# Optimization experiments

Hardware: AMD Instinct MI355X
Metric: run time of the kernel (lower is better)

The kernel has to match this reference:

```python
import jax, jax.numpy as jnp
import numpy as np

N_EVENTS = 50000
TS_SIZE = 512
N_NEURONS = 256
LAMBDA_HOMEO = 0.25


def setup_inputs() -> dict:
    key = jax.random.key(0)
    k1, k2 = jax.random.split(key)
    # event time surfaces (nonnegative, like torch surfaces)
    all_ts = jax.random.uniform(k1, (N_EVENTS, TS_SIZE), dtype=jnp.float32)
    # synapses.weight ~ U[0,1), as in torch.nn.init.uniform_(a=0,b=1)
    W = jax.random.uniform(k2, (N_NEURONS, TS_SIZE), dtype=jnp.float32)
    cumhisto = jnp.ones((N_NEURONS,), dtype=jnp.float32)
    return {"all_ts": all_ts, "W": W, "cumhisto": cumhisto}


def reference(all_ts, W, cumhisto):
    """Training branch (learning_flag=True, homeo_flag=True) of hotslayer.forward.

    Sequential per-event: normalize ts, cosine-like scores beta, homeostatic gain
    picks the winner, winner row of W is pulled toward ts, histogram incremented.
    Returns (per-event winners [N_EVENTS], final W [N,TS], final cumhisto [N]).
    """
    n_neurons = W.shape[0]

    def step(carry, ts):
        W, ch = carry
        ts = ts / jnp.linalg.norm(ts)
        w_norm = jnp.linalg.norm(W, axis=1)          # [N]
        beta = (W @ ts) / w_norm                      # [N]
        gain = jnp.exp(LAMBDA_HOMEO * (1.0 - n_neurons * ch / ch.sum()))
        n_star = jnp.argmax(gain * beta)
        Ck = W[n_star]                                # [TS]
        alpha = 0.01 / (1.0 + ch[n_star] / 20000.0)
        W = W.at[n_star].set(Ck + alpha * beta[n_star] * (ts - Ck))
        ch = ch.at[n_star].add(1.0)
        return (W, ch), n_star

    (W_f, ch_f), winners = jax.lax.scan(step, (W, cumhisto), all_ts)
    return winners, W_f, ch_f
```

## Files before the change

kernel.cpp:

```cpp
#include <hip/hip_runtime.h>
#include <hip/hip_bf16.h>

#define N_EVENTS 50000
#define TS 512
#define NN 256
#define BATCH 512
#define SUB 64
#define LAMB 0.25f
#define NB 98

#define RLF(v, l) __int_as_float(__builtin_amdgcn_readlane(__float_as_int(v), (l)))
#define RLI(v, l) __builtin_amdgcn_readlane((v), (l))
#define FRCP(x) __builtin_amdgcn_rcpf(x)
#define FRSQ(x) __builtin_amdgcn_rsqf(x)
#define DPP_MAXF(x, ctrl)                                                            \
    { int _s = __builtin_amdgcn_update_dpp(__float_as_int(x), __float_as_int(x),     \
                                           (ctrl), 0xF, 0xF, false);                 \
      (x) = fmaxf((x), __int_as_float(_s)); }

typedef unsigned long long u64;


__global__ __launch_bounds__(256)
void inv_kernel(const float* __restrict__ ts, float* __restrict__ inv)
{
    __shared__ double red[256];
    const int e = blockIdx.x;
    const int d = threadIdx.x;
    const float* row = ts + (size_t)e * TS;
    float x0 = row[d], x1 = row[d + 256];
    red[d] = (double)x0 * x0 + (double)x1 * x1;
    __syncthreads();
    for (int st = 128; st > 0; st >>= 1) {
        if (d < st) red[d] += red[d + st];
        __syncthreads();
    }
    if (d == 0) inv[e] = (float)(1.0 / sqrt(red[0]));
}

__global__ __launch_bounds__(256)
void init_kernel(const float* __restrict__ chin, float* __restrict__ ch,
                 float* Pn0, float* Pn1, float* phi0, float* phi1,
                 float* c0, float* c1, float* d0, float* d1,
                 int* w0, int* w1)
{
    int i = blockIdx.x * 256 + threadIdx.x;
    if (i < NN) { ch[i] = chin[i]; Pn0[i] = 1.f; Pn1[i] = 1.f; }
    if (i < BATCH) {
        phi0[i] = 0.f; phi1[i] = 0.f; c0[i] = 0.f; c1[i] = 0.f;
        d0[i] = 0.f; d1[i] = 0.f; w0[i] = 0; w1[i] = 0;
    }
}


__device__ void gram_tile(float* SH, const float* __restrict__ ts,
                          const float* __restrict__ inv,
                          int astart, int as, int bstart2, int bs2,
                          int be, int bf, float* __restrict__ outp, int transpose)
{
    float* At = SH;
    float* Bt = SH + 64 * 33;
    if (be * 64 >= as || bf * 64 >= bs2) return;
    const int tx = threadIdx.x & 15, ty = threadIdx.x >> 4;
    float acc[4][4] = {};
    for (int kt = 0; kt < TS; kt += 32) {
        for (int it = threadIdx.x; it < 64 * 32; it += 256) {
            int r = it >> 5, c = it & 31;
            int ra = be * 64 + r, rb = bf * 64 + r;
            At[r * 33 + c] = (ra < as) ? ts[(size_t)(astart + ra) * TS + kt + c] : 0.f;
            Bt[r * 33 + c] = (rb < bs2) ? ts[(size_t)(bstart2 + rb) * TS + kt + c] : 0.f;
        }
        __syncthreads();
#pragma unroll
        for (int kk = 0; kk < 32; ++kk) {
            float av[4], bv[4];
#pragma unroll
            for (int i = 0; i < 4; ++i) av[i] = At[(ty * 4 + i) * 33 + kk];
#pragma unroll
            for (int j = 0; j < 4; ++j) bv[j] = Bt[(tx * 4 + j) * 33 + kk];
#pragma unroll
            for (int i = 0; i < 4; ++i)
#pragma unroll
                for (int j = 0; j < 4; ++j)
                    acc[i][j] += av[i] * bv[j];
        }
        __syncthreads();
    }
#pragma unroll
    for (int i = 0; i < 4; ++i) {
        int e = be * 64 + ty * 4 + i;
        if (e >= as) continue;
        float ie = inv[astart + e];
#pragma unroll
        for (int j = 0; j < 4; ++j) {
            int f = bf * 64 + tx * 4 + j;
            if (f >= bs2) continue;
            float v = acc[i][j] * ie * inv[bstart2 + f];
            if (transpose) outp[(size_t)f * BATCH + e] = v;
            else           outp[(size_t)e * BATCH + f] = v;
        }
    }
}

__global__ __launch_bounds__(256)
void gram_kernel(const float* __restrict__ ts, const float* __restrict__ inv,
                 float* __restrict__ outp, int astart, int as, int bstart2, int bs2,
                 int upper, int transpose)
{
    __shared__ float SHg[64 * 33 * 2];
    if (upper && (int)blockIdx.y < (int)blockIdx.x) return;
    gram_tile(SHg, ts, inv, astart, as, bstart2, bs2, blockIdx.x, blockIdx.y,
              outp, transpose);
}


__device__ void neuron_body(float* shf, double* red,
    const float* __restrict__ ts, const float* __restrict__ inv,
    const float* __restrict__ Wsrc, float* __restrict__ wdst,
    const int* __restrict__ winPrev, const float* __restrict__ phiPrev,
    const float* __restrict__ PnPrev,
    float* __restrict__ wn2W, float* __restrict__ S2W,
    const float* __restrict__ chbuf, float* __restrict__ chout,
    int n, int bprev_start, int bs_prev, int bnext_start, int bs_next)
{
    int* winS = (int*)shf;
    float* phiS = shf + 512;
    float* WL = shf + 1024;
    const int d = threadIdx.x;
    for (int i = d; i < bs_prev; i += 256) { winS[i] = winPrev[i]; phiS[i] = phiPrev[i]; }
    __syncthreads();
    const float Pf = PnPrev[n];
    float w0 = Wsrc[n * TS + d];
    float w1 = Wsrc[n * TS + d + 256];
    double a0 = 0.0, a1 = 0.0;
    for (int e = 0; e < bs_prev; ++e) {
        if (winS[e] == n) {
            double coef = (double)phiS[e];
            float iv = inv[bprev_start + e];
            const float* tr = ts + (size_t)(bprev_start + e) * TS;
            a0 += coef * (double)(tr[d] * iv);
            a1 += coef * (double)(tr[d + 256] * iv);
        }
    }
    w0 = (float)((double)Pf * ((double)w0 + a0));
    w1 = (float)((double)Pf * ((double)w1 + a1));
    wdst[n * TS + d] = w0;
    wdst[n * TS + d + 256] = w1;
    WL[d] = w0; WL[d + 256] = w1;
    if (wn2W) {
        red[d] = (double)w0 * w0 + (double)w1 * w1;
        __syncthreads();
        for (int st = 128; st > 0; st >>= 1) {
            if (d < st) red[d] += red[d + st];
            __syncthreads();
        }
        if (d == 0) wn2W[n] = (float)red[0];
    } else {
        __syncthreads();
    }
    if (bs_next > 0) {
#pragma unroll
        for (int rep = 0; rep < 2; ++rep) {
            int f = d + rep * 256;
            if (f < bs_next) {
                double acc = 0.0;
                const float* tr = ts + (size_t)(bnext_start + f) * TS;
                for (int k = 0; k < TS; ++k) acc += (double)tr[k] * (double)WL[k];
                S2W[f * NN + n] = (float)(acc * (double)inv[bnext_start + f]);
            }
        }
    }
    if (chout && d == 0) chout[n] = chbuf[n];
}

__global__ __launch_bounds__(256)
void neuron_kernel(const float* __restrict__ ts, const float* __restrict__ inv,
    const float* __restrict__ Wsrc, float* __restrict__ wdst,
    const int* __restrict__ winPrev, const float* __restrict__ phiPrev,
    const float* __restrict__ PnPrev,
    float* __restrict__ wn2W, float* __restrict__ S2W,
    const float* __restrict__ chbuf, float* __restrict__ chout,
    int bprev_start, int bs_prev, int bnext_start, int bs_next)
{
    __shared__ float SHN[1536];
    __shared__ double redN[256];
    neuron_body(SHN, redN, ts, inv, Wsrc, wdst, winPrev, phiPrev, PnPrev,
                wn2W, S2W, chbuf, chout, blockIdx.x,
                bprev_start, bs_prev, bnext_start, bs_next);
}


__global__ __launch_bounds__(256)
void fix_kernel(const float* __restrict__ S2r, const float* __restrict__ GxTr,
    const int* __restrict__ winPrev, const float* __restrict__ phiPrev,
    const float* __restrict__ cPrev, const float* __restrict__ dPrev,
    const float* __restrict__ PnPrev, const float* __restrict__ wn2b,
    float* __restrict__ S0corr, float* __restrict__ wn2start,
    int bs, int b0flag)
{
    __shared__ int winS[512];
    __shared__ float phiP[512];
    __shared__ float gr[512];
    __shared__ float cS[512];
    __shared__ float dS[512];
    const int tid = threadIdx.x;
    const int f = blockIdx.x;
    for (int i = tid; i < 512; i += 256) {
        int w = winPrev[i];
        winS[i] = w;
        phiP[i] = b0flag ? 0.f : phiPrev[i] * PnPrev[w];
        cS[i] = cPrev[i];
        dS[i] = dPrev[i];
        gr[i] = (b0flag || f >= bs) ? 0.f : GxTr[(size_t)f * BATCH + i];
    }
    __syncthreads();
    if (f < bs) {
        int n = tid;
        float acc = PnPrev[n] * S2r[f * NN + n];
        if (!b0flag) {
            for (int e = 0; e < 512; ++e)
                if (winS[e] == n) acc += phiP[e] * gr[e];
        }
        S0corr[f * NN + n] = acc;
    }
    if (f == 0 && tid < 64) {
        const int lane = tid;
        float w2[4];
#pragma unroll
        for (int k = 0; k < 4; ++k) w2[k] = wn2b[k * 64 + lane];
        for (int e = 0; e < 512; ++e) {
            float c = cS[e];
            if (c != 0.f) {
                int w = winS[e];
                int owner = w & 63, kk = w >> 6;
                float omc = 1.f - c;
                float t2 = 2.f * c * omc * dS[e] + c * c;
#pragma unroll
                for (int k = 0; k < 4; ++k)
                    if (lane == owner && k == kk) w2[k] = omc * omc * w2[k] + t2;
            }
        }
#pragma unroll
        for (int k = 0; k < 4; ++k) wn2start[k * 64 + lane] = w2[k];
    }
}


__device__ void block0_body(float* SH,
    const float* __restrict__ S0corr, const float* __restrict__ GwR,
    const float* __restrict__ wn2start, float* __restrict__ chbuf,
    int* __restrict__ winCur, float* __restrict__ phiCur,
    float* __restrict__ cCur, float* __restrict__ dotCur, float* __restrict__ PnCur,
    float* __restrict__ winners_out, int bstart, int bs)
{
    float* ACC = SH;
    float* GS  = SH + 16384;
    float* GL  = SH + 20480;
    int*   winL = (int*)(SH + 24576);
    float* phiL = SH + 25088;
    float* cL   = SH + 25600;
    float* dL   = SH + 26112;

    const int tid = threadIdx.x, wid = tid >> 6, lane = tid & 63;

    const float KC = -(LAMB * 256.0f * 1.44269504f);
    float ch0 = 0, ch1 = 0, ch2 = 0, ch3 = 0;
    float w20 = 1, w21 = 1, w22 = 1, w23 = 1;
    float rn0 = 1, rn1 = 1, rn2 = 1, rn3 = 1;
    float Pn0 = 1, Pn1 = 1, Pn2 = 1, Pn3 = 1;
    float Sbase = 1.f;
    if (wid == 0) {
        ch0 = chbuf[lane];        ch1 = chbuf[64 + lane];
        ch2 = chbuf[128 + lane];  ch3 = chbuf[192 + lane];
        w20 = wn2start[lane];       w21 = wn2start[64 + lane];
        w22 = wn2start[128 + lane]; w23 = wn2start[192 + lane];
        rn0 = FRSQ(w20); rn1 = FRSQ(w21); rn2 = FRSQ(w22); rn3 = FRSQ(w23);
        float loc = ch0 + ch1 + ch2 + ch3;
#pragma unroll
        for (int off = 32; off > 0; off >>= 1) loc += __shfl_xor(loc, off, 64);
        Sbase = loc;
    }

    const int nsub = (bs + SUB - 1) >> 6;
    for (int sub = 0; sub < nsub; ++sub) {
        const int s0 = sub << 6;
        const int cnt = min(SUB, bs - s0);
        __syncthreads();
        {
            const int n = tid;
            for (int f = 0; f < cnt; f += 8) {
                const float* src = S0corr + (size_t)(s0 + f) * NN + n;
                float v0 = src[0 * NN], v1 = src[1 * NN], v2 = src[2 * NN], v3 = src[3 * NN];
                float v4 = src[4 * NN], v5 = src[5 * NN], v6 = src[6 * NN], v7 = src[7 * NN];
                ACC[(f + 0) * NN + ((n + f + 0) & 255)] = v0;
                ACC[(f + 1) * NN + ((n + f + 1) & 255)] = v1;
                ACC[(f + 2) * NN + ((n + f + 2) & 255)] = v2;
                ACC[(f + 3) * NN + ((n + f + 3) & 255)] = v3;
                ACC[(f + 4) * NN + ((n + f + 4) & 255)] = v4;
                ACC[(f + 5) * NN + ((n + f + 5) & 255)] = v5;
                ACC[(f + 6) * NN + ((n + f + 6) & 255)] = v6;
                ACC[(f + 7) * NN + ((n + f + 7) & 255)] = v7;
            }
        }
        for (int it = tid; it < SUB * SUB; it += 256) {
            int t = it >> 6, f = it & 63;
            GS[it] = (t < cnt && f < cnt) ? GwR[(size_t)(s0 + t) * BATCH + s0 + f] : 0.f;
        }
        for (int base = 0; base < s0; base += 64) {
            {
                const int i0 = tid, i1 = tid + 256, i2 = tid + 512, i3 = tid + 768;
                for (int rep = 0; rep < 4096; rep += 1024) {
                    float g0 = GwR[(size_t)(base + ((i0 + rep) >> 6)) * BATCH + s0 + (i0 & 63)];
                    float g1 = GwR[(size_t)(base + ((i1 + rep) >> 6)) * BATCH + s0 + (i1 & 63)];
                    float g2 = GwR[(size_t)(base + ((i2 + rep) >> 6)) * BATCH + s0 + (i2 & 63)];
                    float g3 = GwR[(size_t)(base + ((i3 + rep) >> 6)) * BATCH + s0 + (i3 & 63)];
                    GL[i0 + rep] = g0; GL[i1 + rep] = g1;
                    GL[i2 + rep] = g2; GL[i3 + rep] = g3;
                }
            }
            int wreg = winL[base + lane];
            float preg = phiL[base + lane];
            __syncthreads();
            for (int j = 0; j < 64; ++j) {
                int wj = RLI(wreg, j);
                if ((wj & 3) == wid) {
                    float pj = RLF(preg, j);
                    if (lane < cnt)
                        ACC[lane * NN + ((wj + lane) & 255)] += pj * GL[j * 64 + lane];
                }
            }
            __syncthreads();
        }
        __syncthreads();

        if (wid == 0) {
            float a0 = ACC[(lane) & 255];
            float a1 = ACC[(64 + lane) & 255];
            float a2 = ACC[(128 + lane) & 255];
            float a3 = ACC[(192 + lane) & 255];

            for (int t = 0; t < cnt; ++t) {
                const int ib = s0 + t;
                const float Kk2 = KC * FRCP(Sbase + (float)ib);
                const bool hn = (t + 1 < cnt);
                const float g1v = GS[t * SUB + ((t + 1) & 63)];
                float n0 = 0.f, n1 = 0.f, n2 = 0.f, n3 = 0.f;
                if (hn) {
                    const int r = t + 1;
                    n0 = ACC[r * NN + ((lane + r) & 255)];
                    n1 = ACC[r * NN + ((64 + lane + r) & 255)];
                    n2 = ACC[r * NN + ((128 + lane + r) & 255)];
                    n3 = ACC[r * NN + ((192 + lane + r) & 255)];
                }
                const int fo = t + 1 + lane;
                const float gval = GS[t * SUB + (fo & 63)];

                const float pa0 = Pn0 * a0, pa1 = Pn1 * a1;
                const float pa2 = Pn2 * a2, pa3 = Pn3 * a3;
                const float b0 = pa0 * rn0, b1 = pa1 * rn1;
                const float b2 = pa2 * rn2, b3 = pa3 * rn3;
                const float k0 = b0 * exp2f(Kk2 * ch0);
                const float k1 = b1 * exp2f(Kk2 * ch1);
                const float k2 = b2 * exp2f(Kk2 * ch2);
                const float k3 = b3 * exp2f(Kk2 * ch3);

                u64 K  = ((u64)(unsigned)__float_as_uint(k0) << 32) | (unsigned)(255 - lane);
                u64 T1 = ((u64)(unsigned)__float_as_uint(k1) << 32) | (unsigned)(191 - lane);
                u64 T2 = ((u64)(unsigned)__float_as_uint(k2) << 32) | (unsigned)(127 - lane);
                u64 T3 = ((u64)(unsigned)__float_as_uint(k3) << 32) | (unsigned)(63 - lane);
                if (T1 > K) K = T1;
                if (T2 > K) K = T2;
                if (T3 > K) K = T3;
#define DPPSTEP(ctrl)                                                              \
                { int _hi = (int)(K >> 32), _lo = (int)(unsigned)K;                 \
                  int _shi = __builtin_amdgcn_update_dpp(_hi, _hi, (ctrl), 0xF, 0xF, false); \
                  int _slo = __builtin_amdgcn_update_dpp(_lo, _lo, (ctrl), 0xF, 0xF, false); \
                  u64 _S = ((u64)(unsigned)_shi << 32) | (unsigned)_slo;           \
                  if (_S > K) K = _S; }
                DPPSTEP(0x111) DPPSTEP(0x112) DPPSTEP(0x114)
                DPPSTEP(0x118) DPPSTEP(0x142) DPPSTEP(0x143)
#undef DPPSTEP
                const int loAll = __builtin_amdgcn_ds_bpermute(63 << 2, (int)(unsigned)K);
                const int ns = 255 - (loAll & 0xFF);
                const int ksq = ns >> 6, owner = ns & 63;

                const float bsel  = (ksq == 0) ? b0  : (ksq == 1) ? b1  : (ksq == 2) ? b2  : b3;
                const float pasel = (ksq == 0) ? pa0 : (ksq == 1) ? pa1 : (ksq == 2) ? pa2 : pa3;
                const float Psel  = (ksq == 0) ? Pn0 : (ksq == 1) ? Pn1 : (ksq == 2) ? Pn2 : Pn3;
                const float csel  = (ksq == 0) ? ch0 : (ksq == 1) ? ch1 : (ksq == 2) ? ch2 : ch3;
                const int oaddr = owner << 2;
                const float betas = __int_as_float(__builtin_amdgcn_ds_bpermute(oaddr, __float_as_int(bsel)));
                const float pas   = __int_as_float(__builtin_amdgcn_ds_bpermute(oaddr, __float_as_int(pasel)));
                const float pold  = __int_as_float(__builtin_amdgcn_ds_bpermute(oaddr, __float_as_int(Psel)));
                const float chs   = __int_as_float(__builtin_amdgcn_ds_bpermute(oaddr, __float_as_int(csel)));

                const float alpha = 0.01f * FRCP(1.0f + chs * (1.0f / 20000.0f));
                const float c    = alpha * betas;
                const float omc  = 1.0f - c;
                const float pnew = pold * omc;
                const float phi  = c * FRCP(pnew);

                const bool lo_own = (lane == owner);
                if (lo_own && ksq == 0) { w20 = omc * omc * w20 + 2.f * c * omc * pas + c * c;
                    rn0 = FRSQ(w20); ch0 += 1.f; Pn0 = pnew; n0 += phi * g1v; }
                if (lo_own && ksq == 1) { w21 = omc * omc * w21 + 2.f * c * omc * pas + c * c;
                    rn1 = FRSQ(w21); ch1 += 1.f; Pn1 = pnew; n1 += phi * g1v; }
                if (lo_own && ksq == 2) { w22 = omc * omc * w22 + 2.f * c * omc * pas + c * c;
                    rn2 = FRSQ(w22); ch2 += 1.f; Pn2 = pnew; n2 += phi * g1v; }
                if (lo_own && ksq == 3) { w23 = omc * omc * w23 + 2.f * c * omc * pas + c * c;
                    rn3 = FRSQ(w23); ch3 += 1.f; Pn3 = pnew; n3 += phi * g1v; }

                if (lane == 0) {
                    winL[ib] = ns; phiL[ib] = phi;
                    cL[ib] = c; dL[ib] = pas;
                }
                if (lane > 0 && fo < cnt)
                    ACC[fo * NN + ((ns + fo) & 255)] += phi * gval;

                if (hn) { a0 = n0; a1 = n1; a2 = n2; a3 = n3; }
            }
        }
    }
    __syncthreads();
    if (wid == 0) {
        chbuf[lane] = ch0;        chbuf[64 + lane] = ch1;
        chbuf[128 + lane] = ch2;  chbuf[192 + lane] = ch3;
        PnCur[lane] = Pn0;        PnCur[64 + lane] = Pn1;
        PnCur[128 + lane] = Pn2;  PnCur[192 + lane] = Pn3;
    }
    for (int i = tid; i < bs; i += 256) {
        int w = winL[i];
        winCur[i] = w;
        phiCur[i] = phiL[i];
        cCur[i] = cL[i];
        dotCur[i] = dL[i];
        winners_out[bstart + i] = (float)w;
    }
}


__global__ __launch_bounds__(256)
void fusedA_kernel(const float* __restrict__ ts, const float* __restrict__ inv,
    const float* __restrict__ S0corr, const float* __restrict__ GwR,
    float* __restrict__ GwW, float* __restrict__ GxTW,
    const float* __restrict__ wn2start, float* __restrict__ chbuf,
    const int* __restrict__ winPrev, const float* __restrict__ phiPrev,
    const float* __restrict__ PnPrev,
    int* __restrict__ winCur, float* __restrict__ phiCur,
    float* __restrict__ cCur, float* __restrict__ dotCur, float* __restrict__ PnCur,
    float* __restrict__ Wcur, float* __restrict__ wn2W, float* __restrict__ S2W,
    float* __restrict__ out, int b, int bstart, int bs, int bnext_start, int bs_next)
{
    __shared__ float SH[26656];
    const int bx = blockIdx.x;
    if (bx == 0) {
        block0_body(SH, S0corr, GwR, wn2start, chbuf,
                    winCur, phiCur, cCur, dotCur, PnCur, out, bstart, bs);
    } else if (bx <= NN) {
        neuron_body(SH, (double*)(SH + 1536), ts, inv, Wcur, Wcur,
                    winPrev, phiPrev, PnPrev, wn2W, S2W, nullptr, nullptr,
                    bx - 1, bstart - BATCH, (b == 0) ? 0 : BATCH,
                    bnext_start, bs_next);
    } else {
        int job = bx - (NN + 1);
        if (bs_next <= 0) return;
        if (job < 64) {
            gram_tile(SH, ts, inv, bstart, bs, bnext_start, bs_next,
                      job >> 3, job & 7, GxTW, 1);
        } else {
            int jw = job - 64;
            int be = 0;
            while (jw >= 8 - be) { jw -= 8 - be; ++be; }
            int bf = be + jw;
            gram_tile(SH, ts, inv, bnext_start, bs_next, bnext_start, bs_next,
                      be, bf, GwW, 0);
        }
    }
}


__global__ __launch_bounds__(256)
void winit_kernel(const float* __restrict__ Wcur, const float* __restrict__ chin,
                  float* __restrict__ ch, float* __restrict__ wn2, float* __restrict__ rn)
{
    __shared__ double red[256];
    const int n = blockIdx.x;
    const int d = threadIdx.x;
    float w0 = Wcur[n * TS + d], w1 = Wcur[n * TS + d + 256];
    red[d] = (double)w0 * w0 + (double)w1 * w1;
    __syncthreads();
    for (int st = 128; st > 0; st >>= 1) {
        if (d < st) red[d] += red[d + st];
        __syncthreads();
    }
    if (d == 0) {
        double s = red[0];
        wn2[n] = (float)s;
        rn[n]  = (float)(1.0 / sqrt(s));
        ch[n]  = chin[n];
    }
}

__global__ __launch_bounds__(256)
void s0_gemm_kernel(const float* __restrict__ ts, const float* __restrict__ Wcur,
                    const float* __restrict__ inv, float* __restrict__ S0P,
                    int bstart, int bs)
{
    __shared__ float At[64][33];
    __shared__ float Bt[64][33];
    const int bf = blockIdx.x;
    const int bn = blockIdx.y;
    if (bf * 64 >= bs) return;
    const int tx = threadIdx.x & 15, ty = threadIdx.x >> 4;
    double acc[4][4] = {};
    for (int kt = 0; kt < TS; kt += 32) {
        for (int it = threadIdx.x; it < 64 * 32; it += 256) {
            int r = it >> 5, c = it & 31;
            int row = bf * 64 + r;
            At[r][c] = (row < bs) ? ts[(size_t)(bstart + row) * TS + kt + c] : 0.f;
            Bt[r][c] = Wcur[(bn * 64 + r) * TS + kt + c];
        }
        __syncthreads();
#pragma unroll
        for (int kk = 0; kk < 32; ++kk) {
            float av[4], bv[4];
#pragma unroll
            for (int i = 0; i < 4; ++i) av[i] = At[ty * 4 + i][kk];
#pragma unroll
            for (int j = 0; j < 4; ++j) bv[j] = Bt[tx * 4 + j][kk];
#pragma unroll
            for (int i = 0; i < 4; ++i)
#pragma unroll
                for (int j = 0; j < 4; ++j)
                    acc[i][j] += (double)av[i] * (double)bv[j];
        }
        __syncthreads();
    }
#pragma unroll
    for (int i = 0; i < 4; ++i) {
        int f = bf * 64 + ty * 4 + i;
        if (f >= bs) continue;
        double iv = (double)inv[bstart + f];
#pragma unroll
        for (int j = 0; j < 4; ++j) {
            int n = bn * 64 + tx * 4 + j;
            S0P[f * NN + n] = (float)(acc[i][j] * iv);
        }
    }
}

__global__ __launch_bounds__(256)
void seq_step_kernel(const float* __restrict__ S0P, const float* __restrict__ Gb,
                     float* __restrict__ ch_g, const float* __restrict__ wn2_g,
                     const float* __restrict__ rn_g, float* __restrict__ Pn_g,
                     float* __restrict__ phi_g, int* __restrict__ win_g,
                     float* __restrict__ winners_out, int bstart, int bs)
{
    __shared__ float ACC[SUB * NN];
    __shared__ float GS[SUB * SUB];
    __shared__ float GL[SUB * SUB];
    __shared__ int   winL[BATCH];
    __shared__ float phiL[BATCH];

    const int tid = threadIdx.x;
    const int wid = tid >> 6;
    const int lane = tid & 63;

    float ch[4] = {0, 0, 0, 0}, wn2v[4] = {1, 1, 1, 1};
    float rn[4] = {1, 1, 1, 1}, Pn[4] = {1, 1, 1, 1};
    float Ssum = 1.f, sinv = 1.f;
    if (wid == 0) {
#pragma unroll
        for (int k = 0; k < 4; ++k) {
            int n = k * 64 + lane;
            ch[k]   = ch_g[n];
            wn2v[k] = wn2_g[n];
            rn[k]   = rn_g[n];
            Pn[k]   = 1.0f;
        }
        float loc = ch[0] + ch[1] + ch[2] + ch[3];
#pragma unroll
        for (int off = 32; off > 0; off >>= 1) loc += __shfl_xor(loc, off, 64);
        Ssum = loc;
        sinv = 1.0f / Ssum;
    }

    const int nsub = (bs + SUB - 1) >> 6;
    for (int sub = 0; sub < nsub; ++sub) {
        const int s0 = sub << 6;
        const int cnt = min(SUB, bs - s0);
        __syncthreads();

        for (int it = tid; it < cnt * NN; it += 256) {
            int r = it >> 8, n = it & 255;
            ACC[r * NN + ((n + r) & 255)] = S0P[(s0 + r) * NN + n];
        }
        for (int it = tid; it < cnt * SUB; it += 256) {
            int t = it >> 6, f = it & 63;
            GS[t * SUB + f] = (f < cnt) ? Gb[(s0 + t) * BATCH + s0 + f] : 0.f;
        }
        __syncthreads();

        for (int base = 0; base < s0; base += 64) {
            for (int it = tid; it < 64 * 64; it += 256)
                GL[it] = Gb[(base + (it >> 6)) * BATCH + s0 + (it & 63)];
            int   wreg = winL[base + lane];
            float preg = phiL[base + lane];
            __syncthreads();
            for (int j = 0; j < 64; ++j) {
                int wj = RLI(wreg, j);
                if ((wj & 3) == wid) {
                    float pj = RLF(preg, j);
                    if (lane < cnt)
                        ACC[lane * NN + ((wj + lane) & 255)] += pj * GL[j * 64 + lane];
                }
            }
            __syncthreads();
        }

        if (wid == 0) {
            float acur[4];
#pragma unroll
            for (int k = 0; k < 4; ++k) acur[k] = ACC[(k * 64 + lane) & 255];

            for (int t = 0; t < cnt; ++t) {
                const bool havenext = (t + 1 < cnt);
                float anext[4] = {0.f, 0.f, 0.f, 0.f};
                if (havenext) {
                    const int r = t + 1;
#pragma unroll
                    for (int k = 0; k < 4; ++k)
                        anext[k] = ACC[r * NN + ((k * 64 + lane + r) & 255)];
                }
                const int forig = t + 1 + lane;
                const float gval = GS[t * SUB + (forig & 63)];

                const float gmul = 256.0f * sinv;
                float beta[4], key[4];
                float kmax;
#pragma unroll
                for (int k = 0; k < 4; ++k) {
                    float dot = Pn[k] * acur[k];
                    beta[k] = dot * rn[k];
                    float frac = ch[k] * gmul;
                    float gain = __expf(LAMB * (1.0f - frac));
                    key[k] = gain * beta[k];
                }
                kmax = fmaxf(fmaxf(key[0], key[1]), fmaxf(key[2], key[3]));
                DPP_MAXF(kmax, 0x111); DPP_MAXF(kmax, 0x112); DPP_MAXF(kmax, 0x114);
                DPP_MAXF(kmax, 0x118); DPP_MAXF(kmax, 0x142); DPP_MAXF(kmax, 0x143);
                const float smax = RLF(kmax, 63);

                unsigned long long m0 = __ballot(key[0] == smax);
                unsigned long long m1 = __ballot(key[1] == smax);
                unsigned long long m2 = __ballot(key[2] == smax);
                unsigned long long m3 = __ballot(key[3] == smax);
                int ns = m0 ? (int)__builtin_ctzll(m0)
                       : m1 ? 64  + (int)__builtin_ctzll(m1)
                       : m2 ? 128 + (int)__builtin_ctzll(m2)
                            : 192 + (int)__builtin_ctzll(m3);
                ns = __builtin_amdgcn_readfirstlane(ns);
                const int owner = ns & 63, ks = ns >> 6;

                float bsel = (ks == 0) ? beta[0] : (ks == 1) ? beta[1] : (ks == 2) ? beta[2] : beta[3];
                float csel = (ks == 0) ? ch[0]   : (ks == 1) ? ch[1]   : (ks == 2) ? ch[2]   : ch[3];
                float asel = (ks == 0) ? acur[0] : (ks == 1) ? acur[1] : (ks == 2) ? acur[2] : acur[3];
                float psel = (ks == 0) ? Pn[0]   : (ks == 1) ? Pn[1]   : (ks == 2) ? Pn[2]   : Pn[3];
                const float betas = RLF(bsel, owner);
                const float chs   = RLF(csel, owner);
                const float dots  = RLF(psel * asel, owner);
                const float pold  = RLF(psel, owner);

                const float alpha = 0.01f / (1.0f + chs / 20000.0f);
                const float c    = alpha * betas;
                const float omc  = 1.0f - c;
                const float pnew = pold * omc;
                const float phi  = c / pnew;
                const float g1   = RLF(gval, 0);

#pragma unroll
                for (int k = 0; k < 4; ++k) {
                    bool me = (lane == owner) && (k == ks);
                    if (me) {
                        wn2v[k] = omc * omc * wn2v[k] + 2.f * c * omc * dots + c * c;
                        rn[k] = 1.0f / sqrtf(wn2v[k]);
                        ch[k] += 1.0f;
                        Pn[k] = pnew;
                        anext[k] += phi * g1;
                    }
                }
                if (lane > 0 && forig < cnt)
                    ACC[forig * NN + ((ns + forig) & 255)] += phi * gval;

                const int ib = s0 + t;
                if (lane == 0) {
                    winL[ib] = ns; phiL[ib] = phi;
                    win_g[ib] = ns; phi_g[ib] = phi;
                    winners_out[bstart + ib] = (float)ns;
                }
                Ssum += 1.0f;
                sinv = 1.0f / Ssum;
                if (havenext) {
#pragma unroll
                    for (int k = 0; k < 4; ++k) acur[k] = anext[k];
                }
            }
        }
        __syncthreads();
    }

    if (wid == 0) {
#pragma unroll
        for (int k = 0; k < 4; ++k) {
            int n = k * 64 + lane;
            ch_g[n] = ch[k];
            Pn_g[n] = Pn[k];
        }
    }
}

__global__ __launch_bounds__(256)
void wupdate_kernel(const float* __restrict__ ts, const float* __restrict__ inv,
                    const int* __restrict__ win_g, const float* __restrict__ phi_g,
                    const float* __restrict__ Pn_g, float* __restrict__ Wcur,
                    float* __restrict__ wn2_g, float* __restrict__ rn_g,
                    int bstart, int bs)
{
    __shared__ int   winS[BATCH];
    __shared__ float phiS[BATCH];
    __shared__ double red[256];
    const int n = blockIdx.x;
    const int d = threadIdx.x;
    for (int i = d; i < bs; i += 256) { winS[i] = win_g[i]; phiS[i] = phi_g[i]; }
    __syncthreads();
    const float Pf = Pn_g[n];
    float w0 = Wcur[n * TS + d];
    float w1 = Wcur[n * TS + d + 256];
    double a0 = 0.0, a1 = 0.0;
    for (int ib = 0; ib < bs; ++ib) {
        if (winS[ib] == n) {
            double coef = (double)phiS[ib] * (double)Pf;
            float iv = inv[bstart + ib];
            const float* tr = ts + (size_t)(bstart + ib) * TS;
            a0 += coef * (double)(tr[d] * iv);
            a1 += coef * (double)(tr[d + 256] * iv);
        }
    }
    w0 = (float)((double)Pf * (double)w0 + a0);
    w1 = (float)((double)Pf * (double)w1 + a1);
    Wcur[n * TS + d] = w0;
    Wcur[n * TS + d + 256] = w1;
    red[d] = (double)w0 * w0 + (double)w1 * w1;
    __syncthreads();
    for (int st = 128; st > 0; st >>= 1) {
        if (d < st) red[d] += red[d + st];
        __syncthreads();
    }
    if (d == 0) {
        double s = red[0];
        wn2_g[n] = (float)s;
        rn_g[n]  = (float)(1.0 / sqrt(s));
    }
}

__global__ __launch_bounds__(256)
void final_kernel(const float* __restrict__ Wcur, const float* __restrict__ ch,
                  float* __restrict__ out)
{
    int i = blockIdx.x * 256 + threadIdx.x;
    if (i < NN * TS) out[N_EVENTS + i] = Wcur[i];
    else if (i < NN * TS + NN) out[N_EVENTS + i] = ch[i - NN * TS];
}


extern "C" void kernel_launch(void* const* d_in, const int* in_sizes, int n_in,
                              void* d_out, int out_size, void* d_ws, size_t ws_size,
                              hipStream_t stream)
{
    const float* ts   = (const float*)d_in[0];
    const float* W0   = (const float*)d_in[1];
    const float* chin = (const float*)d_in[2];
    float* out = (float*)d_out;
    float* ws  = (float*)d_ws;

    const size_t FULL_FLOATS = 1628544;
    if (ws_size >= FULL_FLOATS * sizeof(float)) {
        float* inv  = ws + 0;
        float* Wcur = ws + 50048;
        float* ch   = ws + 181120;
        float* wn2b[2] = { ws + 181376, ws + 181632 };
        float* wn2s = ws + 181888;
        float* Pn[2]  = { ws + 182144, ws + 182400 };
        float* phi[2] = { ws + 182656, ws + 183168 };
        float* cE[2]  = { ws + 183680, ws + 184192 };
        float* dE[2]  = { ws + 184704, ws + 185216 };
        int*   win[2] = { (int*)(ws + 185728), (int*)(ws + 186240) };
        float* S2[2]  = { ws + 186752, ws + 317824 };
        float* S0c    = ws + 448896;
        float* GxT[2] = { ws + 579968, ws + 842112 };
        float* Gw[2]  = { ws + 1104256, ws + 1366400 };

        hipMemcpyAsync(Wcur, W0, (size_t)NN * TS * sizeof(float),
                       hipMemcpyDeviceToDevice, stream);
        inv_kernel<<<N_EVENTS, 256, 0, stream>>>(ts, inv);
        init_kernel<<<2, 256, 0, stream>>>(chin, ch, Pn[0], Pn[1], phi[0], phi[1],
                                           cE[0], cE[1], dE[0], dE[1], win[0], win[1]);
        neuron_kernel<<<NN, 256, 0, stream>>>(ts, inv, Wcur, Wcur,
            win[1], phi[1], Pn[1], wn2b[0], S2[0], nullptr, nullptr,
            0, 0, 0, BATCH);
        gram_kernel<<<dim3(8, 8), 256, 0, stream>>>(ts, inv, Gw[0],
            0, BATCH, 0, BATCH, 1, 0);

        for (int b = 0; b < NB; ++b) {
            const int cs = b & 1, ps = 1 - cs;
            const int bstart = b * BATCH;
            const int bs = min(BATCH, N_EVENTS - bstart);
            const int bnext = bstart + BATCH;
            const int bsn = (b == NB - 1) ? 0 : min(BATCH, N_EVENTS - bnext);

            fix_kernel<<<BATCH, 256, 0, stream>>>(S2[cs], GxT[cs],
                win[ps], phi[ps], cE[ps], dE[ps], Pn[ps], wn2b[cs],
                S0c, wn2s, bs, (b == 0) ? 1 : 0);

            const int grid = (b == NB - 1) ? (NN + 1) : (NN + 1 + 100);
            fusedA_kernel<<<grid, 256, 0, stream>>>(ts, inv, S0c, Gw[cs],
                Gw[ps], GxT[ps], wn2s, ch,
                win[ps], phi[ps], Pn[ps],
                win[cs], phi[cs], cE[cs], dE[cs], Pn[cs],
                Wcur, wn2b[ps], S2[ps],
                out, b, bstart, bs, bnext, bsn);
        }
        neuron_kernel<<<NN, 256, 0, stream>>>(ts, inv, Wcur, out + N_EVENTS,
            win[1], phi[1], Pn[1], nullptr, nullptr, ch, out + N_EVENTS + NN * TS,
            97 * BATCH, 336, 0, 0);
    } else {
        float* inv  = ws + 0;
        float* Wcur = ws + 50048;
        float* ch   = ws + 181120;
        float* wn2  = ws + 181376;
        float* rn   = ws + 181632;
        float* Pn   = ws + 181888;
        float* phi  = ws + 182144;
        int*   win  = (int*)(ws + 182656);
        float* S0P  = ws + 183168;
        float* G    = ws + 314240;

        hipMemcpyAsync(Wcur, W0, (size_t)NN * TS * sizeof(float),
                       hipMemcpyDeviceToDevice, stream);
        inv_kernel<<<N_EVENTS, 256, 0, stream>>>(ts, inv);
        winit_kernel<<<NN, 256, 0, stream>>>(Wcur, chin, ch, wn2, rn);

        for (int b = 0; b < NB; ++b) {
            int bstart = b * BATCH;
            int bs = min(BATCH, N_EVENTS - bstart);
            s0_gemm_kernel<<<dim3(8, 4), 256, 0, stream>>>(ts, Wcur, inv, S0P, bstart, bs);
            gram_kernel<<<dim3(8, 8), 256, 0, stream>>>(ts, inv, G,
                bstart, bs, bstart, bs, 1, 0);
            seq_step_kernel<<<1, 256, 0, stream>>>(S0P, G, ch, wn2, rn, Pn, phi, win,
                                                   out, bstart, bs);
            wupdate_kernel<<<NN, 256, 0, stream>>>(ts, inv, win, phi, Pn, Wcur,
                                                   wn2, rn, bstart, bs);
        }
        final_kernel<<<(NN * TS + NN + 255) / 256, 256, 0, stream>>>(Wcur, ch, out);
    }
}
```

Before: 62.64 ms.

## Defer winner state update via top-2 argmax to shorten the serial dependency chain

The sequential winner-selection loop now tracks the top two keys across the wavefront reduction. The previous winner's update (state writeback and ACC propagation) is applied lazily in the next iteration. The previous winner's new key is recomputed separately and merged with the best key among the other neurons. This takes the per-step state update off the critical path between one argmax and the next, so it can overlap with the reduction. In exchange the DPP reduction work doubles, plus an extra bpermute and more registers and branching.

```diff
diff --git a/kernel.cpp b/kernel.cpp
--- a/kernel.cpp
+++ b/kernel.cpp
@@ -334,27 +334,18 @@
         __syncthreads();
 
         if (wid == 0) {
-            float a0 = ACC[(lane) & 255];
-            float a1 = ACC[(64 + lane) & 255];
-            float a2 = ACC[(128 + lane) & 255];
-            float a3 = ACC[(192 + lane) & 255];
+            int   p = 0;
+            float up_phi = 0.f, up_pnew = 1.f, up_w2 = 1.f, up_rn = 1.f, up_ch = 0.f;
+            float bp_a = 0.f, bp_Pn = 1.f, bp_rn = 1.f, bp_ch = 0.f, bp_w2 = 1.f;
 
             for (int t = 0; t < cnt; ++t) {
                 const int ib = s0 + t;
                 const float Kk2 = KC * FRCP(Sbase + (float)ib);
-                const bool hn = (t + 1 < cnt);
-                const float g1v = GS[t * SUB + ((t + 1) & 63)];
-                float n0 = 0.f, n1 = 0.f, n2 = 0.f, n3 = 0.f;
-                if (hn) {
-                    const int r = t + 1;
-                    n0 = ACC[r * NN + ((lane + r) & 255)];
-                    n1 = ACC[r * NN + ((64 + lane + r) & 255)];
-                    n2 = ACC[r * NN + ((128 + lane + r) & 255)];
-                    n3 = ACC[r * NN + ((192 + lane + r) & 255)];
-                }
-                const int fo = t + 1 + lane;
-                const float gval = GS[t * SUB + (fo & 63)];
-
+
+                const float a0 = ACC[t * NN + ((lane + t) & 255)];
+                const float a1 = ACC[t * NN + ((64 + lane + t) & 255)];
+                const float a2 = ACC[t * NN + ((128 + lane + t) & 255)];
+                const float a3 = ACC[t * NN + ((192 + lane + t) & 255)];
                 const float pa0 = Pn0 * a0, pa1 = Pn1 * a1;
                 const float pa2 = Pn2 * a2, pa3 = Pn3 * a3;
                 const float b0 = pa0 * rn0, b1 = pa1 * rn1;
@@ -363,61 +354,105 @@
                 const float k1 = b1 * exp2f(Kk2 * ch1);
                 const float k2 = b2 * exp2f(Kk2 * ch2);
                 const float k3 = b3 * exp2f(Kk2 * ch3);
-
-                u64 K  = ((u64)(unsigned)__float_as_uint(k0) << 32) | (unsigned)(255 - lane);
-                u64 T1 = ((u64)(unsigned)__float_as_uint(k1) << 32) | (unsigned)(191 - lane);
-                u64 T2 = ((u64)(unsigned)__float_as_uint(k2) << 32) | (unsigned)(127 - lane);
-                u64 T3 = ((u64)(unsigned)__float_as_uint(k3) << 32) | (unsigned)(63 - lane);
-                if (T1 > K) K = T1;
-                if (T2 > K) K = T2;
-                if (T3 > K) K = T3;
-#define DPPSTEP(ctrl)                                                              \
-                { int _hi = (int)(K >> 32), _lo = (int)(unsigned)K;                 \
-                  int _shi = __builtin_amdgcn_update_dpp(_hi, _hi, (ctrl), 0xF, 0xF, false); \
-                  int _slo = __builtin_amdgcn_update_dpp(_lo, _lo, (ctrl), 0xF, 0xF, false); \
-                  u64 _S = ((u64)(unsigned)_shi << 32) | (unsigned)_slo;           \
-                  if (_S > K) K = _S; }
-                DPPSTEP(0x111) DPPSTEP(0x112) DPPSTEP(0x114)
-                DPPSTEP(0x118) DPPSTEP(0x142) DPPSTEP(0x143)
-#undef DPPSTEP
-                const int loAll = __builtin_amdgcn_ds_bpermute(63 << 2, (int)(unsigned)K);
-                const int ns = 255 - (loAll & 0xFF);
-                const int ksq = ns >> 6, owner = ns & 63;
+                u64 Q0 = ((u64)(unsigned)__float_as_uint(k0) << 32) | (unsigned)(255 - lane);
+                u64 Q1 = ((u64)(unsigned)__float_as_uint(k1) << 32) | (unsigned)(191 - lane);
+                u64 Q2 = ((u64)(unsigned)__float_as_uint(k2) << 32) | (unsigned)(127 - lane);
+                u64 Q3 = ((u64)(unsigned)__float_as_uint(k3) << 32) | (unsigned)(63 - lane);
+                u64 M1 = Q0, M2 = Q1;
+                if (M2 > M1) { u64 tm = M1; M1 = M2; M2 = tm; }
+                if (Q2 > M1) { M2 = M1; M1 = Q2; } else if (Q2 > M2) M2 = Q2;
+                if (Q3 > M1) { M2 = M1; M1 = Q3; } else if (Q3 > M2) M2 = Q3;
+#define DPPD(ctrl) { \
+    int s1h = __builtin_amdgcn_update_dpp((int)(M1 >> 32), (int)(M1 >> 32), (ctrl), 0xF, 0xF, false); \
+    int s1l = __builtin_amdgcn_update_dpp((int)(unsigned)M1, (int)(unsigned)M1, (ctrl), 0xF, 0xF, false); \
+    int s2h = __builtin_amdgcn_update_dpp((int)(M2 >> 32), (int)(M2 >> 32), (ctrl), 0xF, 0xF, false); \
+    int s2l = __builtin_amdgcn_update_dpp((int)(unsigned)M2, (int)(unsigned)M2, (ctrl), 0xF, 0xF, false); \
+    u64 S1 = ((u64)(unsigned)s1h << 32) | (unsigned)s1l; \
+    u64 S2 = ((u64)(unsigned)s2h << 32) | (unsigned)s2l; \
+    if (S1 == M1)      { M2 = (M2 > S2) ? M2 : S2; } \
+    else if (S1 > M1)  { M2 = (M1 > S2) ? M1 : S2; M1 = S1; } \
+    else               { M2 = (S1 > M2) ? S1 : M2; } }
+                DPPD(0x111) DPPD(0x112) DPPD(0x114)
+                DPPD(0x118) DPPD(0x142) DPPD(0x143)
+#undef DPPD
+
+                if (t > 0) {
+                    const bool own = (lane == (p & 63));
+                    const int pq = p >> 6;
+                    if (own && pq == 0) { Pn0 = up_pnew; w20 = up_w2; rn0 = up_rn; ch0 = up_ch; }
+                    if (own && pq == 1) { Pn1 = up_pnew; w21 = up_w2; rn1 = up_rn; ch1 = up_ch; }
+                    if (own && pq == 2) { Pn2 = up_pnew; w22 = up_w2; rn2 = up_rn; ch2 = up_ch; }
+                    if (own && pq == 3) { Pn3 = up_pnew; w23 = up_w2; rn3 = up_rn; ch3 = up_ch; }
+                    const int fo2 = t + lane;
+                    if (lane > 0 && fo2 < cnt) {
+                        const float gv = GS[(t - 1) * SUB + (fo2 & 63)];
+                        ACC[fo2 * NN + ((p + fo2) & 255)] += up_phi * gv;
+                    }
+                }
+
+                u64 Wk;
+                float pap = 0.f, beta_p = 0.f;
+                if (t > 0) {
+                    pap = bp_Pn * bp_a;
+                    beta_p = pap * bp_rn;
+                    const float key_p = beta_p * exp2f(Kk2 * bp_ch);
+                    u64 Kp = ((u64)(unsigned)__float_as_uint(key_p) << 32) | (unsigned)(255 - p);
+                    const int n1 = 255 - (int)(M1 & 0xFFull);
+                    u64 excl = (n1 == p) ? M2 : M1;
+                    Wk = (excl > Kp) ? excl : Kp;
+                } else {
+                    Wk = M1;
+                }
+                const int wlo = __builtin_amdgcn_ds_bpermute(63 << 2, (int)(unsigned)Wk);
+                const int ns = 255 - (wlo & 0xFF);
+                const int ksq = ns >> 6;
+                const int oaddr = (ns & 63) << 2;
 
                 const float bsel  = (ksq == 0) ? b0  : (ksq == 1) ? b1  : (ksq == 2) ? b2  : b3;
                 const float pasel = (ksq == 0) ? pa0 : (ksq == 1) ? pa1 : (ksq == 2) ? pa2 : pa3;
                 const float Psel  = (ksq == 0) ? Pn0 : (ksq == 1) ? Pn1 : (ksq == 2) ? Pn2 : Pn3;
                 const float csel  = (ksq == 0) ? ch0 : (ksq == 1) ? ch1 : (ksq == 2) ? ch2 : ch3;
-                const int oaddr = owner << 2;
-                const float betas = __int_as_float(__builtin_amdgcn_ds_bpermute(oaddr, __float_as_int(bsel)));
-                const float pas   = __int_as_float(__builtin_amdgcn_ds_bpermute(oaddr, __float_as_int(pasel)));
-                const float pold  = __int_as_float(__builtin_amdgcn_ds_bpermute(oaddr, __float_as_int(Psel)));
-                const float chs   = __int_as_float(__builtin_amdgcn_ds_bpermute(oaddr, __float_as_int(csel)));
+                const float wsel  = (ksq == 0) ? w20 : (ksq == 1) ? w21 : (ksq == 2) ? w22 : w23;
+                const float Bb  = __int_as_float(__builtin_amdgcn_ds_bpermute(oaddr, __float_as_int(bsel)));
+                const float Bpa = __int_as_float(__builtin_amdgcn_ds_bpermute(oaddr, __float_as_int(pasel)));
+                const float BPn = __int_as_float(__builtin_amdgcn_ds_bpermute(oaddr, __float_as_int(Psel)));
+                const float Bch = __int_as_float(__builtin_amdgcn_ds_bpermute(oaddr, __float_as_int(csel)));
+                const float Bw2 = __int_as_float(__builtin_amdgcn_ds_bpermute(oaddr, __float_as_int(wsel)));
+                const bool isp = (t > 0) && (ns == p);
+                const float betas = isp ? beta_p : Bb;
+                const float pas   = isp ? pap    : Bpa;
+                const float pold  = isp ? bp_Pn  : BPn;
+                const float chs   = isp ? bp_ch  : Bch;
+                const float w2s   = isp ? bp_w2  : Bw2;
 
                 const float alpha = 0.01f * FRCP(1.0f + chs * (1.0f / 20000.0f));
-                const float c    = alpha * betas;
-                const float omc  = 1.0f - c;
-                const float pnew = pold * omc;
-                const float phi  = c * FRCP(pnew);
-
-                const bool lo_own = (lane == owner);
-                if (lo_own && ksq == 0) { w20 = omc * omc * w20 + 2.f * c * omc * pas + c * c;
-                    rn0 = FRSQ(w20); ch0 += 1.f; Pn0 = pnew; n0 += phi * g1v; }
-                if (lo_own && ksq == 1) { w21 = omc * omc * w21 + 2.f * c * omc * pas + c * c;
-                    rn1 = FRSQ(w21); ch1 += 1.f; Pn1 = pnew; n1 += phi * g1v; }
-                if (lo_own && ksq == 2) { w22 = omc * omc * w22 + 2.f * c * omc * pas + c * c;
-                    rn2 = FRSQ(w22); ch2 += 1.f; Pn2 = pnew; n2 += phi * g1v; }
-                if (lo_own && ksq == 3) { w23 = omc * omc * w23 + 2.f * c * omc * pas + c * c;
-                    rn3 = FRSQ(w23); ch3 += 1.f; Pn3 = pnew; n3 += phi * g1v; }
+                const float c     = alpha * betas;
+                const float omc   = 1.0f - c;
+                const float pnew  = pold * omc;
+                const float phi   = c * FRCP(pnew);
+                const float w2n   = omc * omc * w2s + 2.f * c * omc * pas + c * c;
+                const float rnn   = FRSQ(w2n);
 
                 if (lane == 0) {
                     winL[ib] = ns; phiL[ib] = phi;
                     cL[ib] = c; dL[ib] = pas;
                 }
-                if (lane > 0 && fo < cnt)
-                    ACC[fo * NN + ((ns + fo) & 255)] += phi * gval;
-
-                if (hn) { a0 = n0; a1 = n1; a2 = n2; a3 = n3; }
+                if (t + 1 < cnt) {
+                    const float av = ACC[(t + 1) * NN + ((ns + t + 1) & 255)];
+                    const float g1 = GS[t * SUB + ((t + 1) & 63)];
+                    bp_a = av + phi * g1;
+                    bp_Pn = pnew; bp_rn = rnn; bp_ch = chs + 1.f; bp_w2 = w2n;
+                }
+                p = ns;
+                up_phi = phi; up_pnew = pnew; up_w2 = w2n; up_rn = rnn; up_ch = chs + 1.f;
+            }
+            {
+                const bool own = (lane == (p & 63));
+                const int pq = p >> 6;
+                if (own && pq == 0) { Pn0 = up_pnew; w20 = up_w2; rn0 = up_rn; ch0 = up_ch; }
+                if (own && pq == 1) { Pn1 = up_pnew; w21 = up_w2; rn1 = up_rn; ch1 = up_ch; }
+                if (own && pq == 2) { Pn2 = up_pnew; w22 = up_w2; rn2 = up_rn; ch2 = up_ch; }
+                if (own && pq == 3) { Pn3 = up_pnew; w23 = up_w2; rn3 = up_rn; ch3 = up_ch; }
             }
         }
     }
```

Result: slower. 83.10 ms (+32.6%).
